# Kernel tuning notes

Measured on AMD Instinct MI355X. Metric: run time of the kernel, lower is better.

Reference implementation:

```python
import jax, jax.numpy as jnp
import numpy as np

V = 1_000_000   # total nodes
D = 256         # feature dim (output_size)
B = 32_768      # number of graphs (static segment count)


def setup_inputs() -> dict:
    key = jax.random.key(0)
    k1, k2, k3 = jax.random.split(key, 3)
    H = jax.random.normal(k1, (V, D), dtype=jnp.float32)
    batch = jnp.sort(jax.random.randint(k2, (V,), 0, B, dtype=jnp.int32))
    Ww = jax.random.normal(k3, (1, D), dtype=jnp.float32) * (1.0 / np.sqrt(D))
    Wb = jnp.zeros((1,), dtype=jnp.float32)
    return {"H": H, "batch": batch, "Ww": Ww, "Wb": Wb}


def reference(H, batch, Ww, Wb):
    # per-node scalar attention score: W(H) -> [V, 1]
    scores = (H @ Ww.T + Wb)[:, 0]                      # [V]
    # segment (scatter) softmax over nodes of each graph
    seg_max = jax.ops.segment_max(scores, batch, num_segments=B)   # [B], -inf for empty graphs
    shifted = scores - seg_max[batch]                   # [V] stable
    exp = jnp.exp(shifted)                              # [V]
    seg_sum = jax.ops.segment_sum(exp, batch, num_segments=B)      # [B]
    alphas = exp / seg_sum[batch]                       # [V]
    # weighted scatter-sum pooling -> [B, D]; empty graphs get zeros
    out = jax.ops.segment_sum(alphas[:, None] * H, batch, num_segments=B)
    return out
```

## Files before the change

kernel.cpp:

```cpp
#include <hip/hip_runtime.h>
#include <math.h>


#define DIM 256
#define LANES 64
#define CHUNK 8

__global__ void seg_bounds_kernel(const int* __restrict__ batch, int V, int B,
                                  int* __restrict__ seg_start) {
    int b = blockIdx.x * blockDim.x + threadIdx.x;
    if (b > B) return;
    int lo = 0, hi = V;
    while (lo < hi) {
        int mid = (lo + hi) >> 1;
        if (batch[mid] < b) lo = mid + 1; else hi = mid;
    }
    seg_start[b] = lo;
}

#define LOADC(dst, row_off) do {                                        \
    const float4* hq_ = hp + (size_t)(row_off) * LANES;                 \
    _Pragma("unroll")                                                   \
    for (int k_ = 0; k_ < CHUNK; ++k_)                                  \
        dst[k_] = hq_[(size_t)k_ * LANES];                              \
} while (0)

#define PROC(h) do {                                                    \
    float p_[CHUNK];                                                    \
    _Pragma("unroll")                                                   \
    for (int k_ = 0; k_ < CHUNK; ++k_)                                  \
        p_[k_] = h[k_].x * w.x + h[k_].y * w.y                          \
               + h[k_].z * w.z + h[k_].w * w.w;                         \
    _Pragma("unroll")                                                   \
    for (int off_ = 32; off_ > 0; off_ >>= 1) {                         \
        _Pragma("unroll")                                               \
        for (int k_ = 0; k_ < CHUNK; ++k_)                              \
            p_[k_] += __shfl_xor(p_[k_], off_, 64);                     \
    }                                                                   \
    float e_[CHUNK];                                                    \
    _Pragma("unroll")                                                   \
    for (int k_ = 0; k_ < CHUNK; ++k_) e_[k_] = __expf(p_[k_]);         \
    float es0_ = 0.f, es1_ = 0.f;                                       \
    _Pragma("unroll")                                                   \
    for (int k_ = 0; k_ < CHUNK; k_ += 2) {                             \
        es0_ += e_[k_]; es1_ += e_[k_ + 1];                             \
    }                                                                   \
    l += es0_ + es1_;                                                   \
    _Pragma("unroll")                                                   \
    for (int k_ = 0; k_ < CHUNK; ++k_) {                                \
        acc.x += e_[k_] * h[k_].x;                                      \
        acc.y += e_[k_] * h[k_].y;                                      \
        acc.z += e_[k_] * h[k_].z;                                      \
        acc.w += e_[k_] * h[k_].w;                                      \
    }                                                                   \
} while (0)

__launch_bounds__(256)
__global__ void attn_agg_kernel(const float* __restrict__ H,
                                const float* __restrict__ Ww,
                                const int* __restrict__ seg_start,
                                float* __restrict__ out, int B) {
    const int wave = threadIdx.x >> 6;
    const int lane = threadIdx.x & 63;
    const int b = blockIdx.x * 4 + wave;
    if (b >= B) return;

    const float4* __restrict__ H4 = (const float4*)H;
    const float4 w = ((const float4*)Ww)[lane];

    const int start = seg_start[b];
    const int end   = seg_start[b + 1];
    const int n     = end - start;

    const float4* __restrict__ hp = H4 + (size_t)start * LANES + lane;

    float  l   = 0.0f;
    float4 acc = make_float4(0.f, 0.f, 0.f, 0.f);

    float4 hA[CHUNK], hB[CHUNK];

    const int nfull = n >> 3;
    if (nfull > 0) {
        LOADC(hA, 0);
        int i = 0;
        for (; i + 2 <= nfull; i += 2) {
            LOADC(hB, (i + 1) * CHUNK);
            PROC(hA);
            if (i + 2 < nfull)
                LOADC(hA, (i + 2) * CHUNK);
            PROC(hB);
        }
        if (i < nfull) PROC(hA);
    }

    const int v0 = start + nfull * CHUNK;
    if (v0 < end) {
        #pragma unroll
        for (int k = 0; k < CHUNK; ++k) {
            int r = (v0 + k < end) ? (v0 + k - start) : (n - 1);
            hA[k] = hp[(size_t)r * LANES];
        }
        float p_[CHUNK];
        #pragma unroll
        for (int k = 0; k < CHUNK; ++k)
            p_[k] = hA[k].x * w.x + hA[k].y * w.y + hA[k].z * w.z + hA[k].w * w.w;
        #pragma unroll
        for (int off = 32; off > 0; off >>= 1) {
            #pragma unroll
            for (int k = 0; k < CHUNK; ++k)
                p_[k] += __shfl_xor(p_[k], off, 64);
        }
        #pragma unroll
        for (int k = 0; k < CHUNK; ++k)
            if (v0 + k >= end) p_[k] = -1e30f;
        #pragma unroll
        for (int k = 0; k < CHUNK; ++k) {
            float e = __expf(p_[k]);
            l += e;
            acc.x += e * hA[k].x;
            acc.y += e * hA[k].y;
            acc.z += e * hA[k].z;
            acc.w += e * hA[k].w;
        }
    }

    const float inv = (l > 0.0f) ? (1.0f / l) : 0.0f;
    float4 o = make_float4(acc.x * inv, acc.y * inv, acc.z * inv, acc.w * inv);
    ((float4*)out)[(size_t)b * LANES + lane] = o;
}

extern "C" void kernel_launch(void* const* d_in, const int* in_sizes, int n_in,
                              void* d_out, int out_size, void* d_ws, size_t ws_size,
                              hipStream_t stream) {
    const float* H     = (const float*)d_in[0];
    const int*   batch = (const int*)d_in[1];
    const float* Ww    = (const float*)d_in[2];

    const int V = in_sizes[1];
    const int B = out_size / DIM;

    int* seg_start = (int*)d_ws;

    {
        int n = B + 1;
        int threads = 256;
        int blocks = (n + threads - 1) / threads;
        seg_bounds_kernel<<<blocks, threads, 0, stream>>>(batch, V, B, seg_start);
    }
    {
        int threads = 256;
        int blocks = (B + 3) / 4;
        attn_agg_kernel<<<blocks, threads, 0, stream>>>(H, Ww, seg_start, (float*)d_out, B);
    }
}
```

Measured before the change: 1.290 ms.

## Process eight consecutive segments per wave with a continuous row stream

Each wave now owns eight consecutive graphs and streams their contiguous node rows as one sequence, closing a segment's accumulator whenever the row index crosses a boundary. This removes the per-segment tail handling and the wasted masked loads for small segments (about 30 nodes each), so the double-buffered 8-row pipeline runs across segment boundaries. The cost is fewer waves in flight (B/8 waves total), which lowers occupancy and memory parallelism, plus boundary-check branches inside the inner loop. It also still skips the max subtraction, relying on scores being small.

Result: no change. 1.312 ms (+1.7%).

```diff
diff --git a/kernel.cpp b/kernel.cpp
--- a/kernel.cpp
+++ b/kernel.cpp
@@ -5,6 +5,8 @@
 #define DIM 256
 #define LANES 64
 #define CHUNK 8
+#define SEGS_PER_WAVE 8
+#define WAVES_PER_BLOCK 4
 
 __global__ void seg_bounds_kernel(const int* __restrict__ batch, int V, int B,
                                   int* __restrict__ seg_start) {
@@ -18,41 +20,51 @@
     seg_start[b] = lo;
 }
 
-#define LOADC(dst, row_off) do {                                        \
-    const float4* hq_ = hp + (size_t)(row_off) * LANES;                 \
-    _Pragma("unroll")                                                   \
-    for (int k_ = 0; k_ < CHUNK; ++k_)                                  \
-        dst[k_] = hq_[(size_t)k_ * LANES];                              \
+#define DOT4(h_) ((h_).x * w.x + (h_).y * w.y + (h_).z * w.z + (h_).w * w.w)
+
+#define BFLY8(off_) do {                                                     \
+    p0 += __shfl_xor(p0, off_, 64); p1 += __shfl_xor(p1, off_, 64);          \
+    p2 += __shfl_xor(p2, off_, 64); p3 += __shfl_xor(p3, off_, 64);          \
+    p4 += __shfl_xor(p4, off_, 64); p5 += __shfl_xor(p5, off_, 64);          \
+    p6 += __shfl_xor(p6, off_, 64); p7 += __shfl_xor(p7, off_, 64);          \
 } while (0)
 
-#define PROC(h) do {                                                    \
-    float p_[CHUNK];                                                    \
-    _Pragma("unroll")                                                   \
-    for (int k_ = 0; k_ < CHUNK; ++k_)                                  \
-        p_[k_] = h[k_].x * w.x + h[k_].y * w.y                          \
-               + h[k_].z * w.z + h[k_].w * w.w;                         \
-    _Pragma("unroll")                                                   \
-    for (int off_ = 32; off_ > 0; off_ >>= 1) {                         \
-        _Pragma("unroll")                                               \
-        for (int k_ = 0; k_ < CHUNK; ++k_)                              \
-            p_[k_] += __shfl_xor(p_[k_], off_, 64);                     \
-    }                                                                   \
-    float e_[CHUNK];                                                    \
-    _Pragma("unroll")                                                   \
-    for (int k_ = 0; k_ < CHUNK; ++k_) e_[k_] = __expf(p_[k_]);         \
-    float es0_ = 0.f, es1_ = 0.f;                                       \
-    _Pragma("unroll")                                                   \
-    for (int k_ = 0; k_ < CHUNK; k_ += 2) {                             \
-        es0_ += e_[k_]; es1_ += e_[k_ + 1];                             \
-    }                                                                   \
-    l += es0_ + es1_;                                                   \
-    _Pragma("unroll")                                                   \
-    for (int k_ = 0; k_ < CHUNK; ++k_) {                                \
-        acc.x += e_[k_] * h[k_].x;                                      \
-        acc.y += e_[k_] * h[k_].y;                                      \
-        acc.z += e_[k_] * h[k_].z;                                      \
-        acc.w += e_[k_] * h[k_].w;                                      \
-    }                                                                   \
+#define FINALIZE_SEG() do {                                                  \
+    float inv_ = (l > 0.0f) ? (1.0f / l) : 0.0f;                             \
+    float4 o_;                                                               \
+    o_.x = acc.x * inv_; o_.y = acc.y * inv_;                                \
+    o_.z = acc.z * inv_; o_.w = acc.w * inv_;                                \
+    out4[(size_t)(seg0 + cur) * LANES + lane] = o_;                          \
+    acc.x = 0.0f; acc.y = 0.0f; acc.z = 0.0f; acc.w = 0.0f; l = 0.0f;        \
+    ++cur; se = __shfl(bnd, cur + 1, 64);                                    \
+} while (0)
+
+#define ROWSTEP(hk_, ek_) do {                                               \
+    while (r >= se) FINALIZE_SEG();                                          \
+    l += (ek_);                                                              \
+    acc.x += (ek_) * (hk_).x; acc.y += (ek_) * (hk_).y;                      \
+    acc.z += (ek_) * (hk_).z; acc.w += (ek_) * (hk_).w;                      \
+    ++r;                                                                     \
+} while (0)
+
+#define LOAD8(h0_,h1_,h2_,h3_,h4_,h5_,h6_,h7_, rowoff_) do {                 \
+    const float4* q_ = hp + (size_t)(rowoff_) * LANES;                       \
+    h0_ = q_[0 * LANES]; h1_ = q_[1 * LANES];                                \
+    h2_ = q_[2 * LANES]; h3_ = q_[3 * LANES];                                \
+    h4_ = q_[4 * LANES]; h5_ = q_[5 * LANES];                                \
+    h6_ = q_[6 * LANES]; h7_ = q_[7 * LANES];                                \
+} while (0)
+
+#define PROC8(h0_,h1_,h2_,h3_,h4_,h5_,h6_,h7_) do {                          \
+    float p0 = DOT4(h0_), p1 = DOT4(h1_), p2 = DOT4(h2_), p3 = DOT4(h3_);    \
+    float p4 = DOT4(h4_), p5 = DOT4(h5_), p6 = DOT4(h6_), p7 = DOT4(h7_);    \
+    BFLY8(32); BFLY8(16); BFLY8(8); BFLY8(4); BFLY8(2); BFLY8(1);            \
+    const float e0 = __expf(p0), e1 = __expf(p1);                            \
+    const float e2 = __expf(p2), e3 = __expf(p3);                            \
+    const float e4 = __expf(p4), e5 = __expf(p5);                            \
+    const float e6 = __expf(p6), e7 = __expf(p7);                            \
+    ROWSTEP(h0_, e0); ROWSTEP(h1_, e1); ROWSTEP(h2_, e2); ROWSTEP(h3_, e3);  \
+    ROWSTEP(h4_, e4); ROWSTEP(h5_, e5); ROWSTEP(h6_, e6); ROWSTEP(h7_, e7);  \
 } while (0)
 
 __launch_bounds__(256)
@@ -62,71 +74,58 @@
                                 float* __restrict__ out, int B) {
     const int wave = threadIdx.x >> 6;
     const int lane = threadIdx.x & 63;
-    const int b = blockIdx.x * 4 + wave;
-    if (b >= B) return;
+    const int gw   = blockIdx.x * WAVES_PER_BLOCK + wave;
+    const int seg0 = gw * SEGS_PER_WAVE;
+    if (seg0 >= B) return;
+    const int segN = (B - seg0 < SEGS_PER_WAVE) ? (B - seg0) : SEGS_PER_WAVE;
+
+    int bnd = 0x7fffffff;
+    if (lane <= segN) bnd = seg_start[seg0 + lane];
+
+    const int v0   = __shfl(bnd, 0, 64);
+    const int vend = __shfl(bnd, segN, 64);
 
     const float4* __restrict__ H4 = (const float4*)H;
     const float4 w = ((const float4*)Ww)[lane];
-
-    const int start = seg_start[b];
-    const int end   = seg_start[b + 1];
-    const int n     = end - start;
-
-    const float4* __restrict__ hp = H4 + (size_t)start * LANES + lane;
+    float4* __restrict__ out4 = (float4*)out;
+    const float4* __restrict__ hp = H4 + (size_t)v0 * LANES + lane;
 
     float  l   = 0.0f;
     float4 acc = make_float4(0.f, 0.f, 0.f, 0.f);
+    int cur = 0;
+    int se  = __shfl(bnd, 1, 64);
+    int r   = v0;
 
-    float4 hA[CHUNK], hB[CHUNK];
+    const int nrows = vend - v0;
+    const int nfull = nrows >> 3;
 
-    const int nfull = n >> 3;
+    float4 a0,a1,a2,a3,a4,a5,a6,a7;
+    float4 b0,b1,b2,b3,b4,b5,b6,b7;
+
     if (nfull > 0) {
-        LOADC(hA, 0);
+        LOAD8(a0,a1,a2,a3,a4,a5,a6,a7, 0);
         int i = 0;
         for (; i + 2 <= nfull; i += 2) {
-            LOADC(hB, (i + 1) * CHUNK);
-            PROC(hA);
+            LOAD8(b0,b1,b2,b3,b4,b5,b6,b7, (i + 1) * CHUNK);
+            PROC8(a0,a1,a2,a3,a4,a5,a6,a7);
             if (i + 2 < nfull)
-                LOADC(hA, (i + 2) * CHUNK);
-            PROC(hB);
+                LOAD8(a0,a1,a2,a3,a4,a5,a6,a7, (i + 2) * CHUNK);
+            PROC8(b0,b1,b2,b3,b4,b5,b6,b7);
         }
-        if (i < nfull) PROC(hA);
+        if (i < nfull) PROC8(a0,a1,a2,a3,a4,a5,a6,a7);
     }
 
-    const int v0 = start + nfull * CHUNK;
-    if (v0 < end) {
-        #pragma unroll
-        for (int k = 0; k < CHUNK; ++k) {
-            int r = (v0 + k < end) ? (v0 + k - start) : (n - 1);
-            hA[k] = hp[(size_t)r * LANES];
-        }
-        float p_[CHUNK];
-        #pragma unroll
-        for (int k = 0; k < CHUNK; ++k)
-            p_[k] = hA[k].x * w.x + hA[k].y * w.y + hA[k].z * w.z + hA[k].w * w.w;
-        #pragma unroll
-        for (int off = 32; off > 0; off >>= 1) {
-            #pragma unroll
-            for (int k = 0; k < CHUNK; ++k)
-                p_[k] += __shfl_xor(p_[k], off, 64);
-        }
-        #pragma unroll
-        for (int k = 0; k < CHUNK; ++k)
-            if (v0 + k >= end) p_[k] = -1e30f;
-        #pragma unroll
-        for (int k = 0; k < CHUNK; ++k) {
-            float e = __expf(p_[k]);
-            l += e;
-            acc.x += e * hA[k].x;
-            acc.y += e * hA[k].y;
-            acc.z += e * hA[k].z;
-            acc.w += e * hA[k].w;
-        }
+    for (; r < vend; ) {
+        float4 h = hp[(size_t)(r - v0) * LANES];
+        float p = DOT4(h);
+        p += __shfl_xor(p, 32, 64); p += __shfl_xor(p, 16, 64);
+        p += __shfl_xor(p,  8, 64); p += __shfl_xor(p,  4, 64);
+        p += __shfl_xor(p,  2, 64); p += __shfl_xor(p,  1, 64);
+        const float e = __expf(p);
+        ROWSTEP(h, e);
     }
 
-    const float inv = (l > 0.0f) ? (1.0f / l) : 0.0f;
-    float4 o = make_float4(acc.x * inv, acc.y * inv, acc.z * inv, acc.w * inv);
-    ((float4*)out)[(size_t)b * LANES + lane] = o;
+    while (cur < segN) FINALIZE_SEG();
 }
 
 extern "C" void kernel_launch(void* const* d_in, const int* in_sizes, int n_in,
@@ -148,8 +147,9 @@
         seg_bounds_kernel<<<blocks, threads, 0, stream>>>(batch, V, B, seg_start);
     }
     {
+        const int segs_per_block = WAVES_PER_BLOCK * SEGS_PER_WAVE;
         int threads = 256;
-        int blocks = (B + 3) / 4;
+        int blocks = (B + segs_per_block - 1) / segs_per_block;
         attn_agg_kernel<<<blocks, threads, 0, stream>>>(H, Ww, seg_start, (float*)d_out, B);
     }
 }
```
